# Performance work log

Measured on AMD Instinct MI355X. Metric: run time of the kernel, lower is better.

## Reference

```python
import jax, jax.numpy as jnp
import numpy as np

V = 100000   # nodes (atoms)
E = 400000   # directed edges (bonds x2)
N = 74       # node_feat_size
NE = 12      # edge_feat_size
G = 200      # graph_feat_size
L = 2        # num_layers - 1 GNN layers
OUT = 1      # output_size
NG = 4000    # molecules in the batch


def _lin_init(k, fan_in, fan_out):
    s = 1.0 / np.sqrt(fan_in)
    return jax.random.uniform(k, (fan_in, fan_out), jnp.float32, -s, s)


def setup_inputs() -> dict:
    key = jax.random.key(0)
    ks = list(jax.random.split(key, 40))
    p = {}
    # node feats uniform in (0.05, 0.95) so mask = 1/(sum(h[:,-4:])*(1-h[:,0])) - 1 is finite
    p["node_feats"] = jax.random.uniform(ks[0], (V, N), jnp.float32, 0.05, 0.95)
    p["edge_feats"] = jax.random.normal(ks[1], (E, NE), jnp.float32)
    # GetContext params
    p["pn_W"] = _lin_init(ks[2], N, G);            p["pn_b"] = jnp.zeros((G,), jnp.float32)
    p["pe1_W"] = _lin_init(ks[3], N + NE, G);      p["pe1_b"] = jnp.zeros((G,), jnp.float32)
    p["pe2_W"] = _lin_init(ks[4], 2 * G, 1);       p["pe2_b"] = jnp.zeros((1,), jnp.float32)
    p["et_W"] = _lin_init(ks[5], G, G);            p["et_b"] = jnp.zeros((G,), jnp.float32)
    p["gru0_Wih"] = _lin_init(ks[6], G, 3 * G);    p["gru0_Whh"] = _lin_init(ks[7], G, 3 * G)
    p["gru0_bih"] = jnp.zeros((3 * G,), jnp.float32)
    p["gru0_bhh"] = jnp.zeros((3 * G,), jnp.float32)
    # stacked GNNLayer params
    p["gnn_pe_W"] = jnp.stack([_lin_init(ks[8 + l], 2 * G, 1) for l in range(L)])
    p["gnn_pe_b"] = jnp.zeros((L, 1), jnp.float32)
    p["gnn_pn_W"] = jnp.stack([_lin_init(ks[10 + l], G, G) for l in range(L)])
    p["gnn_pn_b"] = jnp.zeros((L, G), jnp.float32)
    p["gnn_gru_Wih"] = jnp.stack([_lin_init(ks[12 + l], G, 3 * G) for l in range(L)])
    p["gnn_gru_Whh"] = jnp.stack([_lin_init(ks[14 + l], G, 3 * G) for l in range(L)])
    p["gnn_gru_bih"] = jnp.zeros((L, 3 * G), jnp.float32)
    p["gnn_gru_bhh"] = jnp.zeros((L, 3 * G), jnp.float32)
    p["pred_W"] = _lin_init(ks[16], G, OUT);       p["pred_b"] = jnp.zeros((OUT,), jnp.float32)
    # graph structure
    p["src"] = jax.random.randint(ks[17], (E,), 0, V)
    p["dst"] = jax.random.randint(ks[18], (E,), 0, V)
    p["graph_ids"] = jnp.arange(V, dtype=jnp.int32) // (V // NG)  # sorted, balanced, non-empty
    p["n_graphs"] = NG
    return p


def _edge_softmax(logits, dst, num_nodes):
    # softmax over incoming edges of each destination node (DGL edge_softmax)
    m = jax.ops.segment_max(logits, dst, num_segments=num_nodes)
    e = jnp.exp(logits - m[dst])
    s = jax.ops.segment_sum(e, dst, num_segments=num_nodes)
    return e / s[dst]


def _gru_cell(x, h, Wih, Whh, bih, bhh):
    gi = x @ Wih + bih
    gh = h @ Whh + bhh
    ir, iz, inn = jnp.split(gi, 3, axis=-1)
    hr, hz, hn = jnp.split(gh, 3, axis=-1)
    r = jax.nn.sigmoid(ir + hr)
    z = jax.nn.sigmoid(iz + hz)
    n = jnp.tanh(inn + r * hn)
    return (1.0 - z) * n + z * h


def _forward(node_feats, edge_feats, pn_W, pn_b, pe1_W, pe1_b, pe2_W, pe2_b,
             et_W, et_b, gru0_Wih, gru0_Whh, gru0_bih, gru0_bhh,
             gnn_pe_W, gnn_pe_b, gnn_pn_W, gnn_pn_b,
             gnn_gru_Wih, gnn_gru_Whh, gnn_gru_bih, gnn_gru_bhh,
             pred_W, pred_b, src, dst, graph_ids, n_graphs):
    Vn = node_feats.shape[0]
    lrelu = jax.nn.leaky_relu  # slope 0.01, matches torch default
    # mask from original node features g.ndata['h']
    mask = jnp.sum(node_feats[:, -4:], axis=1) * (1.0 - node_feats[:, 0])
    mask = 1.0 / mask - 1.0
    # --- GetContext ---
    hv_new = lrelu(node_feats @ pn_W + pn_b)                               # (V, G)
    he1 = lrelu(jnp.concatenate([node_feats[src], edge_feats], 1) @ pe1_W + pe1_b)  # (E, G)
    he2 = jnp.concatenate([hv_new[dst], he1], 1)                           # (E, 2G)
    logits = lrelu(he2 @ pe2_W + pe2_b)                                    # (E, 1)
    a = _edge_softmax(logits, dst, Vn)
    e = a * (he1 @ et_W + et_b)                                            # (E, G)
    c = jax.ops.segment_sum(e, dst, num_segments=Vn)                       # (V, G)
    nf = jax.nn.relu(_gru_cell(jax.nn.elu(c), hv_new,
                               gru0_Wih, gru0_Whh, gru0_bih, gru0_bhh))
    # --- GNN layers ---
    for l in range(gnn_pe_W.shape[0]):
        he = jnp.concatenate([nf[dst], nf[src]], 1)                        # (E, 2G)
        lg = lrelu(he @ gnn_pe_W[l] + gnn_pe_b[l])                         # (E, 1)
        a = _edge_softmax(lg, dst, Vn)
        hvp = nf @ gnn_pn_W[l] + gnn_pn_b[l]                               # (V, G)
        c = jax.ops.segment_sum(hvp[src] * a, dst, num_segments=Vn)        # (V, G)
        nf = jax.nn.relu(_gru_cell(jax.nn.elu(c), nf,
                                   gnn_gru_Wih[l], gnn_gru_Whh[l],
                                   gnn_gru_bih[l], gnn_gru_bhh[l]))
    # --- readout ---
    atom_pka = nf @ pred_W + pred_b                                        # (V, 1)
    atom_pka = -(atom_pka + mask[:, None])
    h_pow = jnp.power(10.0, atom_pka)
    g_feats = -jnp.log10(jax.ops.segment_sum(h_pow, graph_ids, num_segments=n_graphs))
    atom_pka_out = -atom_pka
    return g_feats, atom_pka_out


def reference(node_feats, edge_feats, pn_W, pn_b, pe1_W, pe1_b, pe2_W, pe2_b,
              et_W, et_b, gru0_Wih, gru0_Whh, gru0_bih, gru0_bhh,
              gnn_pe_W, gnn_pe_b, gnn_pn_W, gnn_pn_b,
              gnn_gru_Wih, gnn_gru_Whh, gnn_gru_bih, gnn_gru_bhh,
              pred_W, pred_b, src, dst, graph_ids, n_graphs):
    return _forward(node_feats, edge_feats, pn_W, pn_b, pe1_W, pe1_b, pe2_W, pe2_b,
                    et_W, et_b, gru0_Wih, gru0_Whh, gru0_bih, gru0_bhh,
                    gnn_pe_W, gnn_pe_b, gnn_pn_W, gnn_pn_b,
                    gnn_gru_Wih, gnn_gru_Whh, gnn_gru_bih, gnn_gru_bhh,
                    pred_W, pred_b, src, dst, graph_ids, n_graphs)
```

## Files before the change

### kernel.cpp

```cpp
#include <hip/hip_runtime.h>
#include <hip/hip_bf16.h>
#include <math.h>

#define V_N    100000
#define E_N    400000
#define NFEAT  74
#define NEFEAT 12
#define G_DIM  200
#define LDA    224
#define L_N    2
#define NG_N   4000
#define NROWB  391
#define NROWP  392
#define NSWZ   (NROWP / 8 * 56)
#define NSWZG  (NROWP / 8 * 112)

static inline int cdiv(int a, int b) { return (a + b - 1) / b; }

__device__ __forceinline__ float lrelu_f(float x) { return x > 0.f ? x : 0.01f * x; }
__device__ __forceinline__ float sigmoid_f(float x)
{
    return __builtin_amdgcn_rcpf(1.f + __expf(-x));
}
__device__ __forceinline__ float tanh_f(float x)
{
    return 1.f - 2.f * __builtin_amdgcn_rcpf(__expf(2.f * x) + 1.f);
}
__device__ __forceinline__ float elu_f(float x) { return x > 0.f ? x : __expf(x) - 1.f; }
__device__ __forceinline__ float bf2f(__hip_bfloat16 x) { return __bfloat162float(x); }
__device__ __forceinline__ float bfbits2f(short s) {
    return __uint_as_float(((unsigned)(unsigned short)s) << 16);
}

__device__ __forceinline__ short f2bf(float f) {
    __hip_bfloat16 b = __float2bfloat16(f);
    short s;
    __builtin_memcpy(&s, &b, 2);
    return s;
}

typedef short short8 __attribute__((ext_vector_type(8)));
typedef short short4v __attribute__((ext_vector_type(4)));
typedef float f32x4 __attribute__((ext_vector_type(4)));

#define MFMA16(a, b, c) __builtin_amdgcn_mfma_f32_16x16x32_bf16((a), (b), (c), 0, 0, 0)

#define GLOAD_LDS16(gp, lp) \
    __builtin_amdgcn_global_load_lds((const __attribute__((address_space(1))) void*)(gp), \
                                     (__attribute__((address_space(3))) void*)(lp), 16, 0, 0)

#define WAITVM(n) do { \
    asm volatile("s_waitcnt vmcnt(" #n ")" ::: "memory"); \
    __builtin_amdgcn_sched_barrier(0); \
} while (0)

__device__ __forceinline__ void swz_decode7(int lin, int& rowBlk, int& cb)
{
    int grp = lin / 56;
    int rem = lin % 56;
    cb = rem >> 3;
    rowBlk = grp * 8 + (rem & 7);
}

__device__ __forceinline__ void swz_decode14(int lin, int& rowBlk, int& cb)
{
    int grp = lin / 112;
    int rem = lin % 112;
    cb = rem >> 3;
    rowBlk = grp * 8 + (rem & 7);
}

__device__ __forceinline__ f32x4 qcalc(const f32x4* wef, f32x4 ef0, f32x4 ef1, f32x4 ef2)
{
    f32x4 q = ef0[0] * wef[0];
    q += ef0[1] * wef[1];
    q += ef0[2] * wef[2];
    q += ef0[3] * wef[3];
    q += ef1[0] * wef[4];
    q += ef1[1] * wef[5];
    q += ef1[2] * wef[6];
    q += ef1[3] * wef[7];
    q += ef2[0] * wef[8];
    q += ef2[1] * wef[9];
    q += ef2[2] * wef[10];
    q += ef2[3] * wef[11];
    return q;
}

__global__ __launch_bounds__(256)
void fill_kernel(float* __restrict__ p, float v, int n)
{
    int i = blockIdx.x * blockDim.x + threadIdx.x;
    if (i < n) p[i] = v;
}

__global__ __launch_bounds__(256)
void fill_int_kernel(int* __restrict__ p, int v, int n)
{
    int i = blockIdx.x * blockDim.x + threadIdx.x;
    if (i < n) p[i] = v;
}

__global__ __launch_bounds__(256)
void pad_zero_kernel(short* __restrict__ base, size_t VP)
{
    int idx = blockIdx.x * blockDim.x + threadIdx.x;
    if (idx >= 4 * V_N) return;
    int mat = idx / V_N, row = idx % V_N;
    short* p = base + (size_t)mat * VP + (long)row * LDA + G_DIM;
    short8 z = {};
    *(short8*)(p) = z;
    *(short8*)(p + 8) = z;
    *(short8*)(p + 16) = z;
}

__global__ __launch_bounds__(256)
void wprep_kernel(const float* __restrict__ W, short* __restrict__ Wp, int K, int Kpad)
{
    int idx = blockIdx.x * 256 + threadIdx.x;
    if (idx >= 256 * Kpad) return;
    int j = idx / Kpad, k = idx % Kpad;
    float v = (j < G_DIM && k < K) ? W[(long)k * G_DIM + j] : 0.f;
    Wp[idx] = f2bf(v);
}

__global__ __launch_bounds__(256)
void wprep_tiled_kernel(const float* __restrict__ W, short* __restrict__ Wp)
{
    int idx = blockIdx.x * 256 + threadIdx.x;
    if (idx >= 7 * 7 * 1024) return;
    int cb = idx / (7 * 1024);
    int r = idx % (7 * 1024);
    int st = r / 1024;
    int r2 = r % 1024;
    int cc = r2 / 32, kk = r2 % 32;
    int col = cb * 32 + cc, k = st * 32 + kk;
    float v = (col < G_DIM && k < G_DIM) ? W[(long)k * G_DIM + col] : 0.f;
    Wp[idx] = f2bf(v);
}

__global__ __launch_bounds__(256)
void gru_wprep_kernel(const float* __restrict__ Wih, const float* __restrict__ Whh,
                      short* __restrict__ Wp)
{
    int idx = blockIdx.x * 256 + threadIdx.x;
    if (idx >= 14 * 14 * 1536) return;
    int cb = idx / (14 * 1536);
    int r = idx % (14 * 1536);
    int st = r / 1536;
    int r2 = r % 1536;
    int g = r2 / 512;
    int r3 = r2 % 512;
    int cc = r3 / 32, kk = r3 % 32;
    int col = cb * 16 + cc;
    float v = 0.f;
    if (col < G_DIM) {
        if (st < 7) {
            int k = st * 32 + kk;
            if (k < G_DIM) v = Wih[(long)k * (3 * G_DIM) + g * G_DIM + col];
        } else {
            int k = (st - 7) * 32 + kk;
            if (k < G_DIM) v = Whh[(long)k * (3 * G_DIM) + g * G_DIM + col];
        }
    }
    Wp[idx] = f2bf(v);
}

__global__ __launch_bounds__(256)
void hist_kernel(const int* __restrict__ dst, int* __restrict__ deg)
{
    int e = blockIdx.x * blockDim.x + threadIdx.x;
    if (e >= E_N) return;
    atomicAdd(&deg[dst[e]], 1);
}

__global__ __launch_bounds__(256)
void scan1_kernel(const int* __restrict__ deg, int* __restrict__ rp, int* __restrict__ bsum)
{
    __shared__ int s[256];
    int tid = threadIdx.x;
    int v = blockIdx.x * 256 + tid;
    int x = (v < V_N) ? deg[v] : 0;
    s[tid] = x;
    __syncthreads();
    for (int off = 1; off < 256; off <<= 1) {
        int t = (tid >= off) ? s[tid - off] : 0;
        __syncthreads();
        s[tid] += t;
        __syncthreads();
    }
    if (v < V_N) rp[v] = s[tid] - x;
    if (tid == 255) bsum[blockIdx.x] = s[255];
}

__global__ void scan2_kernel(int* __restrict__ bsum, int* __restrict__ rp, int nb)
{
    if (threadIdx.x != 0 || blockIdx.x != 0) return;
    int acc = 0;
    for (int b = 0; b < nb; b++) { int t = bsum[b]; bsum[b] = acc; acc += t; }
    rp[V_N] = acc;
}

__global__ __launch_bounds__(256)
void scan3_kernel(int* __restrict__ rp, const int* __restrict__ bsum)
{
    int v = blockIdx.x * 256 + threadIdx.x;
    if (v < V_N) rp[v] += bsum[v >> 8];
}

__global__ __launch_bounds__(256)
void csr_fill_kernel(const int* __restrict__ dst, const int* __restrict__ src,
                     const int* __restrict__ rp,
                     int* __restrict__ cnt, int2* __restrict__ perm)
{
    int e = blockIdx.x * blockDim.x + threadIdx.x;
    if (e >= E_N) return;
    int d = dst[e];
    int pos = rp[d] + atomicAdd(&cnt[d], 1);
    perm[pos] = make_int2(e, src[e]);
}

__global__ __launch_bounds__(256)
void gemm_f32a_dual_kernel(const float* __restrict__ Af32,
                           const short* __restrict__ Wp1, const float* __restrict__ b1,
                           const short* __restrict__ Wp2, const float* __restrict__ b2,
                           __hip_bfloat16* __restrict__ C1,
                           __hip_bfloat16* __restrict__ C2)
{
    __shared__ short As[64 * 40];
    __shared__ short Bs1[64 * 40];
    __shared__ short Bs2[64 * 40];
    const int tid = threadIdx.x;
    const int lane = tid & 63;
    const int w = tid >> 6;
    const int quad = lane >> 4;
    const int lm = lane & 15;
    const int rowBase = blockIdx.y * 64;
    const int j0 = blockIdx.x * 64;
    const int arow = tid >> 2;
    const int akc = (tid & 3) * 8;
    const int agrow = rowBase + arow;

    f32x4 acc1[4] = {}, acc2[4] = {};

    for (int k0 = 0; k0 < 96; k0 += 32) {
        short8 av = {};
        if (agrow < V_N) {
            int gk = k0 + akc;
            #pragma unroll
            for (int i = 0; i < 8; i++) {
                int kg = gk + i;
                av[i] = (kg < NFEAT) ? f2bf(Af32[(long)agrow * NFEAT + kg]) : (short)0;
            }
        }
        *(short8*)&As[arow * 40 + akc] = av;
        {
            int col = tid >> 2;
            *(short8*)&Bs1[col * 40 + akc] =
                *(const short8*)(Wp1 + (long)(j0 + col) * 96 + k0 + akc);
            *(short8*)&Bs2[col * 40 + akc] =
                *(const short8*)(Wp2 + (long)(j0 + col) * 96 + k0 + akc);
        }
        __syncthreads();
        short8 a = *(short8*)&As[(w * 16 + lm) * 40 + quad * 8];
        #pragma unroll
        for (int nt = 0; nt < 4; nt++) {
            short8 bb1 = *(short8*)&Bs1[(nt * 16 + lm) * 40 + quad * 8];
            short8 bb2 = *(short8*)&Bs2[(nt * 16 + lm) * 40 + quad * 8];
            acc1[nt] = MFMA16(a, bb1, acc1[nt]);
            acc2[nt] = MFMA16(a, bb2, acc2[nt]);
        }
        __syncthreads();
    }

    #pragma unroll
    for (int nt = 0; nt < 4; nt++) {
        int col = j0 + nt * 16 + lm;
        if (col >= G_DIM) continue;
        float bv1 = b1[col], bv2 = b2[col];
        #pragma unroll
        for (int r = 0; r < 4; r++) {
            int grow = rowBase + w * 16 + quad * 4 + r;
            if (grow >= V_N) continue;
            C1[(long)grow * LDA + col] = __float2bfloat16(lrelu_f(acc1[nt][r] + bv1));
            C2[(long)grow * LDA + col] = __float2bfloat16(acc2[nt][r] + bv2);
        }
    }
}

template<int EPI>
__global__ __launch_bounds__(256)
void gemm_bf16a_kernel(const __hip_bfloat16* __restrict__ Abf,
                       const short* __restrict__ Wp,
                       const float* __restrict__ bias,
                       __hip_bfloat16* __restrict__ Cbf)
{
    __shared__ short As[2][256 * 32];
    int rowBlk, cb;
    swz_decode7(blockIdx.x, rowBlk, cb);
    if (rowBlk >= NROWB) return;
    const int tid = threadIdx.x;
    const int lane = tid & 63;
    const int w = tid >> 6;
    const int quad = lane >> 4;
    const int lm = lane & 15;
    const int j0 = cb * 32;
    const int rowBase = rowBlk * 256;

    const short* WpB = Wp + (long)cb * (7 * 1024);
    const short* As_g = (const short*)Abf;
    const long aoff = (long)(rowBase + w * 64 + (lane >> 2)) * LDA + (lane & 3) * 8;
    const int bfrag = lm * 32 + quad * 8;

    auto stageA = [&](int st, int buf) {
        const int kl = st * 32;
        #pragma unroll
        for (int c = 0; c < 4; c++)
            GLOAD_LDS16(As_g + aoff + (long)c * 16 * LDA + kl,
                        &As[buf][(w * 64 + c * 16) * 32]);
    };
    auto loadB = [&](int st, short8 bf[2]) {
        const short* bp = WpB + st * 1024 + bfrag;
        #pragma unroll
        for (int nt = 0; nt < 2; nt++)
            bf[nt] = *(const short8*)(bp + nt * 512);
    };
    auto mfmaStep = [&](int buf, short8 bf[2], f32x4 acc[4][2]) {
        #pragma unroll
        for (int rt = 0; rt < 4; rt++) {
            short8 a = *(short8*)&As[buf][(w * 64 + rt * 16 + lm) * 32 + quad * 8];
            acc[rt][0] = MFMA16(a, bf[0], acc[rt][0]);
            acc[rt][1] = MFMA16(a, bf[1], acc[rt][1]);
        }
    };

    f32x4 acc[4][2] = {};
    short8 bA[2], bB[2];

    stageA(0, 0);
    loadB(0, bA);
    WAITVM(0);

    #pragma unroll 1
    for (int st = 0; st < 7; st += 2) {
        if (st + 1 < 7) {
            stageA(st + 1, 1);
            loadB(st + 1, bB);
            WAITVM(6);
        } else {
            WAITVM(0);
        }
        mfmaStep(0, bA, acc);
        if (st + 1 < 7) {
            if (st + 2 < 7) {
                stageA(st + 2, 0);
                loadB(st + 2, bA);
                WAITVM(6);
            } else {
                WAITVM(0);
            }
            mfmaStep(1, bB, acc);
        }
    }

    #pragma unroll
    for (int nt = 0; nt < 2; nt++) {
        int col = j0 + nt * 16 + lm;
        if (col >= G_DIM) continue;
        float bv = bias[col];
        #pragma unroll
        for (int rt = 0; rt < 4; rt++) {
            #pragma unroll
            for (int r = 0; r < 4; r++) {
                int grow = rowBase + w * 64 + rt * 16 + quad * 4 + r;
                if (grow >= V_N) continue;
                float v = acc[rt][nt][r] + bv;
                if (EPI == 3) v = elu_f(v);
                Cbf[(long)grow * LDA + col] = __float2bfloat16(v);
            }
        }
    }
}

__global__ __launch_bounds__(256, 3)
void gru_mfma_kernel(const __hip_bfloat16* __restrict__ xc,
                     const __hip_bfloat16* __restrict__ h,
                     const short* __restrict__ Wp,
                     const float* __restrict__ bih, const float* __restrict__ bhh,
                     __hip_bfloat16* __restrict__ out)
{
    __shared__ short As[2][256 * 32];
    int rowBlk, cb;
    swz_decode14(blockIdx.x, rowBlk, cb);
    if (rowBlk >= NROWB) return;
    const int tid = threadIdx.x;
    const int lane = tid & 63;
    const int w = tid >> 6;
    const int quad = lane >> 4;
    const int lm = lane & 15;
    const int j0 = cb * 16;
    const int rowBase = rowBlk * 256;

    const short* WpB = Wp + (long)cb * (14 * 1536);
    const short* xc_s = (const short*)xc;
    const short* h_s = (const short*)h;
    const long aoff = (long)(rowBase + w * 64 + (lane >> 2)) * LDA + (lane & 3) * 8;
    const int bfrag = lm * 32 + quad * 8;

    auto stageA = [&](int st, int buf) {
        const short* Ap = (st < 7) ? xc_s : h_s;
        const int kl = (st < 7 ? st : st - 7) * 32;
        #pragma unroll
        for (int c = 0; c < 4; c++)
            GLOAD_LDS16(Ap + aoff + (long)c * 16 * LDA + kl,
                        &As[buf][(w * 64 + c * 16) * 32]);
    };
    auto loadB = [&](int st, short8 bf[3]) {
        const short* bp = WpB + st * 1536 + bfrag;
        #pragma unroll
        for (int g = 0; g < 3; g++)
            bf[g] = *(const short8*)(bp + g * 512);
    };

    f32x4 aR[4] = {}, aZ[4] = {}, aNl[4] = {}, aNh[4] = {};

    auto mfmaStep = [&](int buf, short8 bf[3], bool lowK) {
        #pragma unroll
        for (int rt = 0; rt < 4; rt++) {
            short8 a = *(short8*)&As[buf][(w * 64 + rt * 16 + lm) * 32 + quad * 8];
            aR[rt] = MFMA16(a, bf[0], aR[rt]);
            aZ[rt] = MFMA16(a, bf[1], aZ[rt]);
            if (lowK) aNl[rt] = MFMA16(a, bf[2], aNl[rt]);
            else      aNh[rt] = MFMA16(a, bf[2], aNh[rt]);
        }
    };

    short8 bA[3], bB[3];

    stageA(0, 0);
    loadB(0, bA);
    WAITVM(0);

    #pragma unroll 1
    for (int st = 0; st < 14; st += 2) {
        stageA(st + 1, 1);
        loadB(st + 1, bB);
        WAITVM(7);
        mfmaStep(0, bA, st < 7);
        if (st + 2 < 14) {
            stageA(st + 2, 0);
            loadB(st + 2, bA);
            WAITVM(7);
        } else {
            WAITVM(0);
        }
        mfmaStep(1, bB, st + 1 < 7);
    }

    int col = j0 + lm;
    if (col < G_DIM) {
        float b_r = bih[col] + bhh[col];
        float b_z = bih[G_DIM + col] + bhh[G_DIM + col];
        float b_in = bih[2 * G_DIM + col];
        float b_hn = bhh[2 * G_DIM + col];
        #pragma unroll
        for (int rt = 0; rt < 4; rt++) {
            #pragma unroll
            for (int r = 0; r < 4; r++) {
                int grow = rowBase + w * 64 + rt * 16 + quad * 4 + r;
                if (grow >= V_N) continue;
                float rr = sigmoid_f(aR[rt][r] + b_r);
                float zz = sigmoid_f(aZ[rt][r] + b_z);
                float nn = tanh_f(aNl[rt][r] + b_in + rr * (aNh[rt][r] + b_hn));
                float hval = bf2f(h[(long)grow * LDA + col]);
                float o = (1.f - zz) * nn + zz * hval;
                out[(long)grow * LDA + col] = __float2bfloat16(o > 0.f ? o : 0.f);
            }
        }
    }
}

__global__ __launch_bounds__(256)
void node_dot2_kernel(const __hip_bfloat16* __restrict__ X,
                      const float* __restrict__ wa, const float* __restrict__ wb,
                      float* __restrict__ s1, float* __restrict__ s2)
{
    int w = threadIdx.x >> 6, lane = threadIdx.x & 63;
    int v = blockIdx.x * 4 + w;
    if (v >= V_N) return;
    int vlane = (lane < 50) ? lane : 0;
    short4v pv = *(const short4v*)((const short*)X + (long)v * LDA + vlane * 4);
    f32x4 wav = *(const f32x4*)(wa + vlane * 4);
    float a = 0.f, b = 0.f;
    #pragma unroll
    for (int u = 0; u < 4; u++) a += bfbits2f(pv[u]) * wav[u];
    if (wb) {
        f32x4 wbv = *(const f32x4*)(wb + vlane * 4);
        #pragma unroll
        for (int u = 0; u < 4; u++) b += bfbits2f(pv[u]) * wbv[u];
    }
    if (lane >= 50) { a = 0.f; b = 0.f; }
    for (int off = 32; off > 0; off >>= 1) {
        a += __shfl_down(a, off, 64);
        if (wb) b += __shfl_down(b, off, 64);
    }
    if (lane == 0) {
        s1[v] = a;
        if (wb) s2[v] = b;
    }
}

__global__ __launch_bounds__(256)
void ctx_fused_kernel(const __hip_bfloat16* __restrict__ P,
                      const float* __restrict__ efeat,
                      const int2* __restrict__ perm,
                      const int* __restrict__ rp,
                      const float* __restrict__ s1,
                      const float* __restrict__ pe1W,
                      const float* __restrict__ pe2W, const float* __restrict__ pe2b,
                      __hip_bfloat16* __restrict__ hbar)
{
    const int tid = threadIdx.x;
    const int w = tid >> 6, lane = tid & 63;
    const int vlane = (lane < 50) ? lane : 0;
    const int v = __builtin_amdgcn_readfirstlane(blockIdx.x * 4 + w);
    if (v >= V_N) return;
    const int b = __builtin_amdgcn_readfirstlane(rp[v]);
    const int en = __builtin_amdgcn_readfirstlane(rp[v + 1]);
    if (en == b) {
        if (lane < 50) {
            short4v z = {};
            *(short4v*)((short*)hbar + (long)v * LDA + lane * 4) = z;
        }
        return;
    }
    f32x4 wef[12];
    #pragma unroll
    for (int j = 0; j < 12; j++)
        wef[j] = *(const f32x4*)(pe1W + (long)(NFEAT + j) * G_DIM + vlane * 4);
    const f32x4 w2 = *(const f32x4*)(pe2W + G_DIM + vlane * 4);
    const float s1b = s1[v] + pe2b[0];

    float m = -INFINITY, ssum = 0.f;
    f32x4 a = {};
    for (int i = b; i < en; i++) {
        const int2 es = perm[i];
        const int e = __builtin_amdgcn_readfirstlane(es.x);
        const int sN = __builtin_amdgcn_readfirstlane(es.y);
        const f32x4 ef0 = *(const f32x4*)(efeat + (long)e * NEFEAT);
        const f32x4 ef1 = *(const f32x4*)(efeat + (long)e * NEFEAT + 4);
        const f32x4 ef2 = *(const f32x4*)(efeat + (long)e * NEFEAT + 8);
        const short4v pv = *(const short4v*)((const short*)P + (long)sN * LDA + vlane * 4);
        const f32x4 q = qcalc(wef, ef0, ef1, ef2);
        f32x4 he;
        #pragma unroll
        for (int u = 0; u < 4; u++) he[u] = lrelu_f(bfbits2f(pv[u]) + q[u]);
        float dot = he[0] * w2[0] + he[1] * w2[1] + he[2] * w2[2] + he[3] * w2[3];
        if (lane >= 50) dot = 0.f;
        #pragma unroll
        for (int off = 32; off > 0; off >>= 1) dot += __shfl_xor(dot, off, 64);
        const float l = lrelu_f(dot + s1b);
        if (l <= m) {
            const float wgt = __expf(l - m);
            ssum += wgt;
            #pragma unroll
            for (int u = 0; u < 4; u++) a[u] += wgt * he[u];
        } else {
            const float scale = __expf(m - l);
            ssum = ssum * scale + 1.f;
            #pragma unroll
            for (int u = 0; u < 4; u++) a[u] = a[u] * scale + he[u];
            m = l;
        }
    }
    const float inv = __builtin_amdgcn_rcpf(ssum);
    if (lane < 50) {
        short4v o;
        #pragma unroll
        for (int u = 0; u < 4; u++) o[u] = f2bf(a[u] * inv);
        *(short4v*)((short*)hbar + (long)v * LDA + lane * 4) = o;
    }
}

__global__ __launch_bounds__(256)
void gnn_fused_agg_kernel(const __hip_bfloat16* __restrict__ X,
                          const int2* __restrict__ perm,
                          const int* __restrict__ rp,
                          const float* __restrict__ s1, const float* __restrict__ s2,
                          const float* __restrict__ bias,
                          __hip_bfloat16* __restrict__ out)
{
    const int tid = threadIdx.x;
    const int w = tid >> 6, lane = tid & 63;
    const int vlane = (lane < 50) ? lane : 0;
    const int v = __builtin_amdgcn_readfirstlane(blockIdx.x * 4 + w);
    if (v >= V_N) return;
    const int b = __builtin_amdgcn_readfirstlane(rp[v]);
    const int en = __builtin_amdgcn_readfirstlane(rp[v + 1]);
    if (en == b) {
        if (lane < 50) {
            short4v z = {};
            *(short4v*)((short*)out + (long)v * LDA + lane * 4) = z;
        }
        return;
    }
    const float s1v = s1[v] + bias[0];
    float m = -INFINITY, ssum = 0.f;
    f32x4 a = {};
    for (int cb0 = b; cb0 < en; cb0 += 64) {
        int i = cb0 + lane;
        int sL = 0;
        float lv = -INFINITY;
        if (i < en) {
            sL = perm[i].y;
            lv = lrelu_f(s1v + s2[sL]);
        }
        float cm = lv;
        #pragma unroll
        for (int off = 32; off > 0; off >>= 1) cm = fmaxf(cm, __shfl_xor(cm, off, 64));
        const float m_new = fmaxf(m, cm);
        const float scale = __expf(m - m_new);
        ssum *= scale;
        #pragma unroll
        for (int u = 0; u < 4; u++) a[u] *= scale;
        float wgt = (i < en) ? __expf(lv - m_new) : 0.f;
        float ws = wgt;
        #pragma unroll
        for (int off = 32; off > 0; off >>= 1) ws += __shfl_xor(ws, off, 64);
        ssum += ws;
        const int cnt = min(64, en - cb0);
        int sT = __shfl(sL, 0, 64);
        float wT = __shfl(wgt, 0, 64);
        short4v pv = *(const short4v*)((const short*)X + (long)sT * LDA + vlane * 4);
        for (int t = 0; t < cnt; t++) {
            short4v npv;
            float wN;
            if (t + 1 < cnt) {
                int sN = __shfl(sL, t + 1, 64);
                wN = __shfl(wgt, t + 1, 64);
                npv = *(const short4v*)((const short*)X + (long)sN * LDA + vlane * 4);
            }
            #pragma unroll
            for (int u = 0; u < 4; u++)
                a[u] += wT * bfbits2f(pv[u]);
            if (t + 1 < cnt) { pv = npv; wT = wN; }
        }
        m = m_new;
    }
    const float inv = __builtin_amdgcn_rcpf(ssum);
    if (lane < 50) {
        short4v o;
        #pragma unroll
        for (int u = 0; u < 4; u++) o[u] = f2bf(elu_f(a[u] * inv));
        *(short4v*)((short*)out + (long)v * LDA + lane * 4) = o;
    }
}

__global__ __launch_bounds__(256)
void mask_kernel(const float* __restrict__ nfeat, float* __restrict__ mask)
{
    int v = blockIdx.x * blockDim.x + threadIdx.x;
    if (v >= V_N) return;
    const float* row = nfeat + (long)v * NFEAT;
    float s = row[NFEAT - 4] + row[NFEAT - 3] + row[NFEAT - 2] + row[NFEAT - 1];
    float m = s * (1.f - row[0]);
    mask[v] = 1.f / m - 1.f;
}

__global__ __launch_bounds__(256)
void readout_kernel(const __hip_bfloat16* __restrict__ nf, const float* __restrict__ predW,
                    const float* __restrict__ predb, const float* __restrict__ mask,
                    const int* __restrict__ gid, float* __restrict__ out_atom,
                    float* __restrict__ gsum)
{
    int gtid = blockIdx.x * blockDim.x + threadIdx.x;
    int v = gtid >> 6, lane = gtid & 63;
    if (v >= V_N) return;
    int vlane = (lane < 50) ? lane : 0;
    short4v pv = *(const short4v*)((const short*)nf + (long)v * LDA + vlane * 4);
    f32x4 wv = *(const f32x4*)(predW + vlane * 4);
    float acc = 0.f;
    #pragma unroll
    for (int u = 0; u < 4; u++) acc += bfbits2f(pv[u]) * wv[u];
    if (lane >= 50) acc = 0.f;
    for (int off = 32; off > 0; off >>= 1) acc += __shfl_down(acc, off, 64);
    if (lane == 0) {
        float p = acc + predb[0] + mask[v];
        out_atom[v] = p;
        atomicAdd(&gsum[gid[v]], exp10f(-p));
    }
}

__global__ __launch_bounds__(256)
void graph_out_kernel(const float* __restrict__ gsum, float* __restrict__ out_g)
{
    int g = blockIdx.x * blockDim.x + threadIdx.x;
    if (g >= NG_N) return;
    out_g[g] = -log10f(gsum[g]);
}

extern "C" void kernel_launch(void* const* d_in, const int* in_sizes, int n_in,
                              void* d_out, int out_size, void* d_ws, size_t ws_size,
                              hipStream_t stream)
{
    const float* node_feats = (const float*)d_in[0];
    const float* edge_feats = (const float*)d_in[1];
    const float* pn_W  = (const float*)d_in[2];
    const float* pn_b  = (const float*)d_in[3];
    const float* pe1_W = (const float*)d_in[4];
    const float* pe1_b = (const float*)d_in[5];
    const float* pe2_W = (const float*)d_in[6];
    const float* pe2_b = (const float*)d_in[7];
    const float* et_W  = (const float*)d_in[8];
    const float* et_b  = (const float*)d_in[9];
    const float* gru0_Wih = (const float*)d_in[10];
    const float* gru0_Whh = (const float*)d_in[11];
    const float* gru0_bih = (const float*)d_in[12];
    const float* gru0_bhh = (const float*)d_in[13];
    const float* gnn_pe_W = (const float*)d_in[14];
    const float* gnn_pe_b = (const float*)d_in[15];
    const float* gnn_pn_W = (const float*)d_in[16];
    const float* gnn_pn_b = (const float*)d_in[17];
    const float* gnn_gru_Wih = (const float*)d_in[18];
    const float* gnn_gru_Whh = (const float*)d_in[19];
    const float* gnn_gru_bih = (const float*)d_in[20];
    const float* gnn_gru_bhh = (const float*)d_in[21];
    const float* pred_W = (const float*)d_in[22];
    const float* pred_b = (const float*)d_in[23];
    const int* src = (const int*)d_in[24];
    const int* dst = (const int*)d_in[25];
    const int* gid = (const int*)d_in[26];

    float* out_g = (float*)d_out;
    float* out_atom = out_g + NG_N;

    char* base = (char*)d_ws;
    size_t off = 0;
    auto take = [&](size_t bytes) -> void* {
        void* p = base + off;
        off += (bytes + 255) & ~(size_t)255;
        return p;
    };
    const size_t VP = (size_t)V_N * LDA;
    const size_t WPL = (size_t)14 * 14 * 1536;
    float* mask   = (float*)take((size_t)V_N * 4);
    float* s1     = (float*)take((size_t)V_N * 4);
    float* s2     = (float*)take((size_t)V_N * 4);
    float* gsum   = (float*)take((size_t)NG_N * 4);
    __hip_bfloat16* c    = (__hip_bfloat16*)take(VP * 2);
    __hip_bfloat16* hv   = (__hip_bfloat16*)take(VP * 2);
    __hip_bfloat16* nf_a = (__hip_bfloat16*)take(VP * 2);
    __hip_bfloat16* nf_b = (__hip_bfloat16*)take(VP * 2);
    short* WpGru = (short*)take(3 * WPL * 2);
    short* Wp_pn0 = (short*)take((size_t)256 * 96 * 2);
    short* Wp_pe1 = (short*)take((size_t)256 * 96 * 2);
    short* Wp_et  = (short*)take((size_t)7 * 7 * 1024 * 2);
    short* Wp_pn1 = (short*)take((size_t)7 * 7 * 1024 * 2);
    short* Wp_pn2 = (short*)take((size_t)7 * 7 * 1024 * 2);
    int* deg  = (int*)take((size_t)V_N * 4);
    int* cnt  = (int*)take((size_t)V_N * 4);
    int* rp   = (int*)take((size_t)(V_N + 1) * 4);
    int2* perm = (int2*)take((size_t)E_N * 8);
    int* bsum = (int*)take((size_t)512 * 4);
    __hip_bfloat16* P    = nf_a;
    __hip_bfloat16* hbar = nf_b;
    __hip_bfloat16* hvp  = hv;

    if (off > ws_size) {
        fill_kernel<<<cdiv(out_size, 256), 256, 0, stream>>>((float*)d_out, -12345.f, out_size);
        return;
    }

    const int BLK = 256;
    const int nScanBlocks = cdiv(V_N, 256);
    const dim3 gOld(4, cdiv(V_N, 64));
    const int gAgg = cdiv(V_N, 4);

    pad_zero_kernel<<<cdiv(4 * V_N, BLK), BLK, 0, stream>>>((short*)c, VP);

    gru_wprep_kernel<<<cdiv(14 * 14 * 1536, 256), BLK, 0, stream>>>(gru0_Wih, gru0_Whh, WpGru);
    for (int l = 0; l < L_N; l++)
        gru_wprep_kernel<<<cdiv(14 * 14 * 1536, 256), BLK, 0, stream>>>(
            gnn_gru_Wih + (size_t)l * G_DIM * 3 * G_DIM,
            gnn_gru_Whh + (size_t)l * G_DIM * 3 * G_DIM,
            WpGru + (size_t)(l + 1) * WPL);
    wprep_kernel<<<cdiv(256 * 96, 256), BLK, 0, stream>>>(pn_W, Wp_pn0, NFEAT, 96);
    wprep_kernel<<<cdiv(256 * 96, 256), BLK, 0, stream>>>(pe1_W, Wp_pe1, NFEAT, 96);
    wprep_tiled_kernel<<<cdiv(7 * 7 * 1024, 256), BLK, 0, stream>>>(et_W, Wp_et);
    wprep_tiled_kernel<<<cdiv(7 * 7 * 1024, 256), BLK, 0, stream>>>(gnn_pn_W, Wp_pn1);
    wprep_tiled_kernel<<<cdiv(7 * 7 * 1024, 256), BLK, 0, stream>>>(
        gnn_pn_W + (size_t)G_DIM * G_DIM, Wp_pn2);

    mask_kernel<<<cdiv(V_N, BLK), BLK, 0, stream>>>(node_feats, mask);

    fill_int_kernel<<<cdiv(V_N, BLK), BLK, 0, stream>>>(deg, 0, V_N);
    hist_kernel<<<cdiv(E_N, BLK), BLK, 0, stream>>>(dst, deg);
    scan1_kernel<<<nScanBlocks, BLK, 0, stream>>>(deg, rp, bsum);
    scan2_kernel<<<1, 1, 0, stream>>>(bsum, rp, nScanBlocks);
    scan3_kernel<<<nScanBlocks, BLK, 0, stream>>>(rp, bsum);
    fill_int_kernel<<<cdiv(V_N, BLK), BLK, 0, stream>>>(cnt, 0, V_N);
    csr_fill_kernel<<<cdiv(E_N, BLK), BLK, 0, stream>>>(dst, src, rp, cnt, perm);

    gemm_f32a_dual_kernel<<<gOld, BLK, 0, stream>>>(
        node_feats, Wp_pn0, pn_b, Wp_pe1, pe1_b, hv, P);
    node_dot2_kernel<<<gAgg, BLK, 0, stream>>>(hv, pe2_W, nullptr, s1, nullptr);
    ctx_fused_kernel<<<gAgg, BLK, 0, stream>>>(
        P, edge_feats, perm, rp, s1, pe1_W, pe2_W, pe2_b, hbar);
    gemm_bf16a_kernel<3><<<NSWZ, BLK, 0, stream>>>(hbar, Wp_et, et_b, c);
    gru_mfma_kernel<<<NSWZG, BLK, 0, stream>>>(c, hv, WpGru, gru0_bih, gru0_bhh, nf_a);

    __hip_bfloat16* cur = nf_a;
    __hip_bfloat16* nxt = nf_b;
    for (int l = 0; l < L_N; l++) {
        const float* pe_W = gnn_pe_W + (size_t)l * 2 * G_DIM;
        const float* pe_b = gnn_pe_b + l;
        const float* pnB  = gnn_pn_b + (size_t)l * G_DIM;
        const float* bih  = gnn_gru_bih + (size_t)l * 3 * G_DIM;
        const float* bhh  = gnn_gru_bhh + (size_t)l * 3 * G_DIM;
        const short* WpPn = (l == 0) ? Wp_pn1 : Wp_pn2;

        node_dot2_kernel<<<gAgg, BLK, 0, stream>>>(cur, pe_W, pe_W + G_DIM, s1, s2);
        gemm_bf16a_kernel<1><<<NSWZ, BLK, 0, stream>>>(cur, WpPn, pnB, hvp);
        gnn_fused_agg_kernel<<<gAgg, BLK, 0, stream>>>(
            hvp, perm, rp, s1, s2, pe_b, c);
        gru_mfma_kernel<<<NSWZG, BLK, 0, stream>>>(
            c, cur, WpGru + (size_t)(l + 1) * WPL, bih, bhh, nxt);

        __hip_bfloat16* tmp = cur; cur = nxt; nxt = tmp;
    }

    fill_kernel<<<cdiv(NG_N, BLK), BLK, 0, stream>>>(gsum, 0.f, NG_N);
    readout_kernel<<<cdiv(V_N * 64, BLK), BLK, 0, stream>>>(
        cur, pred_W, pred_b, mask, gid, out_atom, gsum);
    graph_out_kernel<<<cdiv(NG_N, BLK), BLK, 0, stream>>>(gsum, out_g);
}
```

Baseline: 1.110 ms.

## Fuse per-node attention dot products into GEMM and GRU epilogues

Removes the separate node_dot2 kernels by computing the per-node dot products with the attention weights inside the epilogues of the dual input GEMM and of the GRU kernels. Partial sums across the 16-column tiles are reduced with lane shuffles and accumulated with float atomics into s1/s2, which must first be zeroed by added fill kernels. This saves re-reading node features and some launches, but adds atomic traffic, extra fill launches, more epilogue work in the register-heavy GRU kernel, and nondeterministic summation order.

```diff
diff --git a/kernel.cpp b/kernel.cpp
--- a/kernel.cpp
+++ b/kernel.cpp
@@ -224,6 +224,7 @@
 void gemm_f32a_dual_kernel(const float* __restrict__ Af32,
                            const short* __restrict__ Wp1, const float* __restrict__ b1,
                            const short* __restrict__ Wp2, const float* __restrict__ b2,
+                           const float* __restrict__ w2, float* __restrict__ s1o,
                            __hip_bfloat16* __restrict__ C1,
                            __hip_bfloat16* __restrict__ C2)
 {
@@ -274,17 +275,26 @@
     }
 
     #pragma unroll
-    for (int nt = 0; nt < 4; nt++) {
-        int col = j0 + nt * 16 + lm;
-        if (col >= G_DIM) continue;
-        float bv1 = b1[col], bv2 = b2[col];
-        #pragma unroll
-        for (int r = 0; r < 4; r++) {
-            int grow = rowBase + w * 16 + quad * 4 + r;
-            if (grow >= V_N) continue;
-            C1[(long)grow * LDA + col] = __float2bfloat16(lrelu_f(acc1[nt][r] + bv1));
-            C2[(long)grow * LDA + col] = __float2bfloat16(acc2[nt][r] + bv2);
-        }
+    for (int r = 0; r < 4; r++) {
+        int grow = rowBase + w * 16 + quad * 4 + r;
+        if (grow >= V_N) continue;
+        float psum = 0.f;
+        #pragma unroll
+        for (int nt = 0; nt < 4; nt++) {
+            int col = j0 + nt * 16 + lm;
+            bool colv = col < G_DIM;
+            int colc = colv ? col : 0;
+            float v1 = lrelu_f(acc1[nt][r] + b1[colc]);
+            float v2 = acc2[nt][r] + b2[colc];
+            if (colv) {
+                C1[(long)grow * LDA + col] = __float2bfloat16(v1);
+                C2[(long)grow * LDA + col] = __float2bfloat16(v2);
+            }
+            psum += colv ? v1 * w2[col] : 0.f;
+        }
+        #pragma unroll
+        for (int off = 1; off < 16; off <<= 1) psum += __shfl_xor(psum, off, 64);
+        if (lm == 0) atomicAdd(&s1o[grow], psum);
     }
 }
 
@@ -387,6 +397,8 @@
                      const __hip_bfloat16* __restrict__ h,
                      const short* __restrict__ Wp,
                      const float* __restrict__ bih, const float* __restrict__ bhh,
+                     const float* __restrict__ wa, const float* __restrict__ wb,
+                     float* __restrict__ s1o, float* __restrict__ s2o,
                      __hip_bfloat16* __restrict__ out)
 {
     __shared__ short As[2][256 * 32];
@@ -457,56 +469,43 @@
         mfmaStep(1, bB, st + 1 < 7);
     }
 
-    int col = j0 + lm;
-    if (col < G_DIM) {
-        float b_r = bih[col] + bhh[col];
-        float b_z = bih[G_DIM + col] + bhh[G_DIM + col];
-        float b_in = bih[2 * G_DIM + col];
-        float b_hn = bhh[2 * G_DIM + col];
-        #pragma unroll
-        for (int rt = 0; rt < 4; rt++) {
-            #pragma unroll
-            for (int r = 0; r < 4; r++) {
-                int grow = rowBase + w * 64 + rt * 16 + quad * 4 + r;
-                if (grow >= V_N) continue;
-                float rr = sigmoid_f(aR[rt][r] + b_r);
-                float zz = sigmoid_f(aZ[rt][r] + b_z);
-                float nn = tanh_f(aNl[rt][r] + b_in + rr * (aNh[rt][r] + b_hn));
-                float hval = bf2f(h[(long)grow * LDA + col]);
-                float o = (1.f - zz) * nn + zz * hval;
-                out[(long)grow * LDA + col] = __float2bfloat16(o > 0.f ? o : 0.f);
+    const int col = j0 + lm;
+    const bool colv = col < G_DIM;
+    const int colc = colv ? col : 0;
+    const float b_r = bih[colc] + bhh[colc];
+    const float b_z = bih[G_DIM + colc] + bhh[G_DIM + colc];
+    const float b_in = bih[2 * G_DIM + colc];
+    const float b_hn = bhh[2 * G_DIM + colc];
+    const bool doDot = (wa != nullptr);
+    const float wav = (doDot && colv) ? wa[col] : 0.f;
+    const float wbv = (doDot && colv) ? wb[col] : 0.f;
+    #pragma unroll
+    for (int rt = 0; rt < 4; rt++) {
+        #pragma unroll
+        for (int r = 0; r < 4; r++) {
+            int grow = rowBase + w * 64 + rt * 16 + quad * 4 + r;
+            if (grow >= V_N) continue;
+            float rr = sigmoid_f(aR[rt][r] + b_r);
+            float zz = sigmoid_f(aZ[rt][r] + b_z);
+            float nn = tanh_f(aNl[rt][r] + b_in + rr * (aNh[rt][r] + b_hn));
+            float hval = bf2f(h[(long)grow * LDA + colc]);
+            float o = (1.f - zz) * nn + zz * hval;
+            float orl = o > 0.f ? o : 0.f;
+            if (colv) out[(long)grow * LDA + col] = __float2bfloat16(orl);
+            if (doDot) {
+                float p1 = orl * wav;
+                float p2 = orl * wbv;
+                #pragma unroll
+                for (int off = 1; off < 16; off <<= 1) {
+                    p1 += __shfl_xor(p1, off, 64);
+                    p2 += __shfl_xor(p2, off, 64);
+                }
+                if (lm == 0) {
+                    atomicAdd(&s1o[grow], p1);
+                    atomicAdd(&s2o[grow], p2);
+                }
             }
         }
-    }
-}
-
-__global__ __launch_bounds__(256)
-void node_dot2_kernel(const __hip_bfloat16* __restrict__ X,
-                      const float* __restrict__ wa, const float* __restrict__ wb,
-                      float* __restrict__ s1, float* __restrict__ s2)
-{
-    int w = threadIdx.x >> 6, lane = threadIdx.x & 63;
-    int v = blockIdx.x * 4 + w;
-    if (v >= V_N) return;
-    int vlane = (lane < 50) ? lane : 0;
-    short4v pv = *(const short4v*)((const short*)X + (long)v * LDA + vlane * 4);
-    f32x4 wav = *(const f32x4*)(wa + vlane * 4);
-    float a = 0.f, b = 0.f;
-    #pragma unroll
-    for (int u = 0; u < 4; u++) a += bfbits2f(pv[u]) * wav[u];
-    if (wb) {
-        f32x4 wbv = *(const f32x4*)(wb + vlane * 4);
-        #pragma unroll
-        for (int u = 0; u < 4; u++) b += bfbits2f(pv[u]) * wbv[u];
-    }
-    if (lane >= 50) { a = 0.f; b = 0.f; }
-    for (int off = 32; off > 0; off >>= 1) {
-        a += __shfl_down(a, off, 64);
-        if (wb) b += __shfl_down(b, off, 64);
-    }
-    if (lane == 0) {
-        s1[v] = a;
-        if (wb) s2[v] = b;
     }
 }
 
@@ -801,30 +800,42 @@
     fill_int_kernel<<<cdiv(V_N, BLK), BLK, 0, stream>>>(cnt, 0, V_N);
     csr_fill_kernel<<<cdiv(E_N, BLK), BLK, 0, stream>>>(dst, src, rp, cnt, perm);
 
+    fill_kernel<<<cdiv(V_N, BLK), BLK, 0, stream>>>(s1, 0.f, V_N);
     gemm_f32a_dual_kernel<<<gOld, BLK, 0, stream>>>(
-        node_feats, Wp_pn0, pn_b, Wp_pe1, pe1_b, hv, P);
-    node_dot2_kernel<<<gAgg, BLK, 0, stream>>>(hv, pe2_W, nullptr, s1, nullptr);
+        node_feats, Wp_pn0, pn_b, Wp_pe1, pe1_b, pe2_W, s1, hv, P);
     ctx_fused_kernel<<<gAgg, BLK, 0, stream>>>(
         P, edge_feats, perm, rp, s1, pe1_W, pe2_W, pe2_b, hbar);
     gemm_bf16a_kernel<3><<<NSWZ, BLK, 0, stream>>>(hbar, Wp_et, et_b, c);
-    gru_mfma_kernel<<<NSWZG, BLK, 0, stream>>>(c, hv, WpGru, gru0_bih, gru0_bhh, nf_a);
+    fill_kernel<<<cdiv(V_N, BLK), BLK, 0, stream>>>(s1, 0.f, V_N);
+    fill_kernel<<<cdiv(V_N, BLK), BLK, 0, stream>>>(s2, 0.f, V_N);
+    gru_mfma_kernel<<<NSWZG, BLK, 0, stream>>>(
+        c, hv, WpGru, gru0_bih, gru0_bhh,
+        gnn_pe_W, gnn_pe_W + G_DIM, s1, s2, nf_a);
 
     __hip_bfloat16* cur = nf_a;
     __hip_bfloat16* nxt = nf_b;
     for (int l = 0; l < L_N; l++) {
-        const float* pe_W = gnn_pe_W + (size_t)l * 2 * G_DIM;
         const float* pe_b = gnn_pe_b + l;
         const float* pnB  = gnn_pn_b + (size_t)l * G_DIM;
         const float* bih  = gnn_gru_bih + (size_t)l * 3 * G_DIM;
         const float* bhh  = gnn_gru_bhh + (size_t)l * 3 * G_DIM;
         const short* WpPn = (l == 0) ? Wp_pn1 : Wp_pn2;
 
-        node_dot2_kernel<<<gAgg, BLK, 0, stream>>>(cur, pe_W, pe_W + G_DIM, s1, s2);
         gemm_bf16a_kernel<1><<<NSWZ, BLK, 0, stream>>>(cur, WpPn, pnB, hvp);
         gnn_fused_agg_kernel<<<gAgg, BLK, 0, stream>>>(
             hvp, perm, rp, s1, s2, pe_b, c);
-        gru_mfma_kernel<<<NSWZG, BLK, 0, stream>>>(
-            c, cur, WpGru + (size_t)(l + 1) * WPL, bih, bhh, nxt);
+        if (l + 1 < L_N) {
+            const float* peN = gnn_pe_W + (size_t)(l + 1) * 2 * G_DIM;
+            fill_kernel<<<cdiv(V_N, BLK), BLK, 0, stream>>>(s1, 0.f, V_N);
+            fill_kernel<<<cdiv(V_N, BLK), BLK, 0, stream>>>(s2, 0.f, V_N);
+            gru_mfma_kernel<<<NSWZG, BLK, 0, stream>>>(
+                c, cur, WpGru + (size_t)(l + 1) * WPL, bih, bhh,
+                peN, peN + G_DIM, s1, s2, nxt);
+        } else {
+            gru_mfma_kernel<<<NSWZG, BLK, 0, stream>>>(
+                c, cur, WpGru + (size_t)(l + 1) * WPL, bih, bhh,
+                nullptr, nullptr, nullptr, nullptr, nxt);
+        }
 
         __hip_bfloat16* tmp = cur; cur = nxt; nxt = tmp;
     }
```

Result: slower. 1.158 ms (+4.3%).
